# Kernel optimization log

Hardware: AMD Instinct MI355X
Metric: run time of the kernel (lower is better)

## Reference

```python
import jax, jax.numpy as jnp
import numpy as np
from jax import lax

B, L, F, D_MODEL = 4, 256, 80, 2048
ED, N, DT_RANK, K, NL = 4096, 16, 2, 4, 6  # d_inner, d_state, dt_rank, d_conv, n_layers


def setup_inputs():
    key = jax.random.key(0)
    ks = jax.random.split(key, 12)
    rn = lambda k, shp, s=0.02: jax.random.normal(k, shp, dtype=jnp.float32) * s
    return {
        "x": jax.random.normal(ks[0], (B, F, L), dtype=jnp.float32),
        "W_emb": rn(ks[1], (F, D_MODEL)),
        "b_emb": jnp.zeros((D_MODEL,), jnp.float32),
        "norm_w": jnp.ones((NL, D_MODEL), jnp.float32),
        "W_in": rn(ks[2], (NL, D_MODEL, 2 * ED)),
        "b_in": jnp.zeros((NL, 2 * ED), jnp.float32),
        "conv_w": rn(ks[3], (NL, ED, K), 0.1),
        "conv_b": jnp.zeros((NL, ED), jnp.float32),
        "W_x": rn(ks[4], (NL, ED, DT_RANK + 2 * N)),
        "W_dt": rn(ks[5], (NL, DT_RANK, ED), 0.1),
        "b_dt": jnp.full((NL, ED), -4.0, jnp.float32),
        "A_log": jnp.tile(jnp.log(jnp.arange(1, N + 1, dtype=jnp.float32))[None, None, :], (NL, ED, 1)),
        "Dp": jnp.ones((NL, ED), jnp.float32),
        "W_out": rn(ks[6], (NL, ED, D_MODEL)),
        "b_out": jnp.zeros((NL, D_MODEL), jnp.float32),
        "W_f": rn(ks[7], (D_MODEL, 1024)),
        "b_f": jnp.zeros((1024,), jnp.float32),
        "W_h1": rn(ks[8], (1024, 512), 0.05),
        "b_h1": jnp.zeros((512,), jnp.float32),
        "W_h2": rn(ks[9], (512, 256), 0.05),
        "b_h2": jnp.zeros((256,), jnp.float32),
        "W_h3": rn(ks[10], (256, 1), 0.05),
        "b_h3": jnp.zeros((1,), jnp.float32),
    }


def _rmsnorm(x, w, eps=1e-5):
    return x * lax.rsqrt(jnp.mean(x * x, axis=-1, keepdims=True) + eps) * w


def _mamba_block(u, W_in, b_in, conv_w, conv_b, W_x, W_dt, b_dt, A_log, Dp, W_out, b_out):
    xz = u @ W_in + b_in                        # (B,L,2*ED)
    xp, z = jnp.split(xz, 2, axis=-1)
    # causal depthwise conv over time, kernel K
    xc = lax.conv_general_dilated(
        xp.transpose(0, 2, 1), conv_w[:, None, :],
        window_strides=(1,), padding=[(K - 1, 0)],
        feature_group_count=ED,
        dimension_numbers=("NCH", "OIH", "NCH")).transpose(0, 2, 1) + conv_b
    xa = jax.nn.silu(xc)                        # (B,L,ED)
    dbc = xa @ W_x                              # (B,L,dt_rank+2N)
    dt = jax.nn.softplus(dbc[..., :DT_RANK] @ W_dt + b_dt)   # (B,L,ED)
    Bm = dbc[..., DT_RANK:DT_RANK + N]
    Cm = dbc[..., DT_RANK + N:]
    A = -jnp.exp(A_log)                         # (ED,N), negative

    def step(h, inp):
        xa_t, dt_t, B_t, C_t = inp
        h = jnp.exp(dt_t[:, :, None] * A) * h + (dt_t * xa_t)[:, :, None] * B_t[:, None, :]
        return h, jnp.einsum("ben,bn->be", h, C_t)

    step = jax.checkpoint(step)
    h0 = jnp.zeros((xa.shape[0], ED, N), xa.dtype)
    _, ys = lax.scan(step, h0, (xa.transpose(1, 0, 2), dt.transpose(1, 0, 2),
                                Bm.transpose(1, 0, 2), Cm.transpose(1, 0, 2)))
    y = ys.transpose(1, 0, 2) + Dp * xa
    y = y * jax.nn.silu(z)
    return y @ W_out + b_out


def reference(x, W_emb, b_emb, norm_w, W_in, b_in, conv_w, conv_b, W_x, W_dt, b_dt, A_log, Dp, W_out, b_out, W_f, b_f, W_h1, b_h1, W_h2, b_h2, W_h3, b_h3):
    h = x.transpose(0, 2, 1) @ W_emb + b_emb    # (B,L,D_MODEL)
    for i in range(NL):
        h = h + _mamba_block(_rmsnorm(h, norm_w[i]), W_in[i], b_in[i], conv_w[i], conv_b[i],
                             W_x[i], W_dt[i], b_dt[i], A_log[i], Dp[i], W_out[i], b_out[i])
    f = h[:, -1] @ W_f + b_f                    # (B,1024)
    g = jax.nn.silu(f @ W_h1 + b_h1)
    g = g @ W_h2 + b_h2
    g = jnp.where(g > 0, g, 0.01 * g)           # LeakyReLU(0.01)
    return jax.nn.sigmoid(g @ W_h3 + b_h3)      # (B,1)
```

## Files before the change

kernel.cpp:

```cpp
#include <hip/hip_runtime.h>
#include <hip/hip_bf16.h>
#include <math.h>

#define D_MODEL 2048
#define EDIM    4096
#define NSTATE  16
#define LSEQ    256
#define BATCH   4
#define NLAYER  6
#define FDIM    80

typedef __attribute__((ext_vector_type(8))) short bf16x8;
typedef __attribute__((ext_vector_type(4))) float f32x4;

__device__ __forceinline__ float silu_f(float x) { return x / (1.f + __expf(-x)); }

__device__ __forceinline__ float softplus_f(float v) {
  return (v > 20.f) ? v : __logf(1.f + __expf(v));
}

__device__ __forceinline__ unsigned short f2bf(float f) {
  unsigned u = __float_as_uint(f);
  unsigned r = u + 0x7fffu + ((u >> 16) & 1u);
  return (unsigned short)(r >> 16);
}

__device__ __forceinline__ float bf2f(unsigned short u) {
  return __uint_as_float((unsigned)u << 16);
}

__device__ __forceinline__ void gload_lds16(const void* g, void* l) {
  __builtin_amdgcn_global_load_lds(
      (const __attribute__((address_space(1))) unsigned int*)g,
      (__attribute__((address_space(3))) unsigned int*)l, 16, 0, 0);
}

__global__ __launch_bounds__(256) void embed_kernel(
    const float* __restrict__ x, const float* __restrict__ W,
    const float* __restrict__ bias, float* __restrict__ h)
{
  int col = blockIdx.x * 256 + threadIdx.x;
  int row = blockIdx.y;
  int b = row >> 8, l = row & 255;
  const float* xp = x + (size_t)b * FDIM * LSEQ + l;
  float acc = bias[col];
  #pragma unroll 8
  for (int f = 0; f < FDIM; ++f)
    acc = fmaf(xp[(size_t)f * LSEQ], W[(size_t)f * D_MODEL + col], acc);
  h[(size_t)row * D_MODEL + col] = acc;
}

__global__ __launch_bounds__(256) void rmsnorm_kernel(
    const float* __restrict__ h, const float* __restrict__ w, unsigned short* __restrict__ u)
{
  int row = blockIdx.x;
  const float* hr = h + (size_t)row * D_MODEL;
  float s = 0.f;
  for (int i = threadIdx.x; i < D_MODEL; i += 256) { float v = hr[i]; s = fmaf(v, v, s); }
  #pragma unroll
  for (int o = 32; o > 0; o >>= 1) s += __shfl_down(s, o);
  __shared__ float red[4];
  int lane = threadIdx.x & 63, wid = threadIdx.x >> 6;
  if (lane == 0) red[wid] = s;
  __syncthreads();
  float total = red[0] + red[1] + red[2] + red[3];
  float scale = rsqrtf(total * (1.f / D_MODEL) + 1e-5f);
  unsigned short* ur = u + (size_t)row * D_MODEL;
  for (int i = threadIdx.x; i < D_MODEL; i += 256) ur[i] = f2bf(hr[i] * scale * w[i]);
}

__global__ __launch_bounds__(256) void wtrans_kernel(
    const float* __restrict__ W, unsigned short* __restrict__ WT, int K, int N)
{
  __shared__ float t[64][65];
  const int k0 = blockIdx.y * 64, n0 = blockIdx.x * 64;
  const int tc = (threadIdx.x & 15) << 2;
  const int tr = threadIdx.x >> 4;
  #pragma unroll
  for (int i = 0; i < 4; ++i) {
    int r = tr + (i << 4);
    float4 v = *(const float4*)(W + (size_t)(k0 + r) * N + n0 + tc);
    t[r][tc + 0] = v.x; t[r][tc + 1] = v.y; t[r][tc + 2] = v.z; t[r][tc + 3] = v.w;
  }
  __syncthreads();
  #pragma unroll
  for (int i = 0; i < 4; ++i) {
    int rr = tr + (i << 4);
    ushort4 o;
    o.x = f2bf(t[tc + 0][rr]);
    o.y = f2bf(t[tc + 1][rr]);
    o.z = f2bf(t[tc + 2][rr]);
    o.w = f2bf(t[tc + 3][rr]);
    *(ushort4*)(WT + (size_t)(n0 + rr) * K + k0 + tc) = o;
  }
}

__global__ __launch_bounds__(256) void wxt_kernel(
    const float* __restrict__ Wx, float* __restrict__ WxT)
{
  const int e = blockIdx.x * 256 + threadIdx.x;
  const int j = blockIdx.y;
  const int l = blockIdx.z;
  WxT[((size_t)l * 34 + j) * EDIM + e] = Wx[(size_t)l * EDIM * 34 + (size_t)e * 34 + j];
}

template<int BN>
__global__ __launch_bounds__(256) void gemm_bf16(
    const unsigned short* __restrict__ A, int lda,
    const unsigned short* __restrict__ BT, int ldb,
    const float* bias,
    const float* resid, int ldr,
    float* __restrict__ C, int ldc, int K)
{
  constexpr int BM = 128;
  constexpr int FN = BN / 32;
  __shared__ unsigned short As[2][BM * 32];
  __shared__ unsigned short Bs[2][BN * 32];
  const int tid  = threadIdx.x;
  const int wave = tid >> 6;
  const int lane = tid & 63;

  const int nwg = gridDim.x * gridDim.y;
  const int cpx = nwg >> 3;
  int flat = blockIdx.y * gridDim.x + blockIdx.x;
  flat = (flat & 7) * cpx + (flat >> 3);
  const int bm = (flat / gridDim.x) * BM;
  const int bn = (flat % gridDim.x) * BN;

  const int wr = (wave >> 1) * 64;
  const int wc = (wave & 1) * (BN / 2);
  const int srow = lane >> 2;
  const int scol = (lane & 3) * 8;

  auto stage = [&](int buf, int k0) {
    #pragma unroll
    for (int i = 0; i < BM / 64; ++i) {
      int c = wave + i * 4;
      gload_lds16(A + (size_t)(bm + c * 16 + srow) * lda + k0 + scol, &As[buf][c * 512]);
    }
    #pragma unroll
    for (int i = 0; i < BN / 64; ++i) {
      int c = wave + i * 4;
      gload_lds16(BT + (size_t)(bn + c * 16 + srow) * ldb + k0 + scol, &Bs[buf][c * 512]);
    }
  };

  f32x4 acc[4][FN];
  #pragma unroll
  for (int m = 0; m < 4; ++m)
    #pragma unroll
    for (int n = 0; n < FN; ++n)
      acc[m][n] = (f32x4){0.f, 0.f, 0.f, 0.f};

  stage(0, 0);
  const int nk = K >> 5;
  for (int t = 0; t < nk; ++t) {
    const int cur = t & 1;
    __syncthreads();
    if (t + 1 < nk) stage(cur ^ 1, (t + 1) << 5);
    bf16x8 af[4], bfr[FN];
    #pragma unroll
    for (int m = 0; m < 4; ++m)
      af[m] = *(const bf16x8*)&As[cur][(wr + m * 16 + (lane & 15)) * 32 + (lane >> 4) * 8];
    #pragma unroll
    for (int n = 0; n < FN; ++n)
      bfr[n] = *(const bf16x8*)&Bs[cur][(wc + n * 16 + (lane & 15)) * 32 + (lane >> 4) * 8];
    #pragma unroll
    for (int m = 0; m < 4; ++m)
      #pragma unroll
      for (int n = 0; n < FN; ++n)
        acc[m][n] = __builtin_amdgcn_mfma_f32_16x16x32_bf16(af[m], bfr[n], acc[m][n], 0, 0, 0);
  }

  const int rbase = (lane >> 4) * 4;
  const int cbase = lane & 15;
  #pragma unroll
  for (int m = 0; m < 4; ++m) {
    #pragma unroll
    for (int n = 0; n < FN; ++n) {
      const int col = bn + wc + n * 16 + cbase;
      const float bv = bias ? bias[col] : 0.f;
      #pragma unroll
      for (int r = 0; r < 4; ++r) {
        const int row = bm + wr + m * 16 + rbase + r;
        float v = acc[m][n][r] + bv;
        if (resid) v += resid[(size_t)row * ldr + col];
        C[(size_t)row * ldc + col] = v;
      }
    }
  }
}

__global__ __launch_bounds__(256) void conv_dbc_kernel(
    const float* __restrict__ xz, const float* __restrict__ cw,
    const float* __restrict__ cb, const float* __restrict__ WxT,
    unsigned short* __restrict__ xab, float* __restrict__ dbc)
{
  const int row = blockIdx.x;
  const int l = row & (LSEQ - 1);
  const int tid = threadIdx.x;
  float a[16];
  const float* base_row = xz + (size_t)row * 8192;
  #pragma unroll
  for (int k = 0; k < 16; ++k) {
    const int e = k * 256 + tid;
    float4 w = *(const float4*)(cw + (size_t)e * 4);
    const float* base = base_row + e;
    float v = cb[e];
    v = fmaf(w.w, base[0], v);
    if (l >= 1) v = fmaf(w.z, base[-8192], v);
    if (l >= 2) v = fmaf(w.y, base[-2 * 8192], v);
    if (l >= 3) v = fmaf(w.x, base[-3 * 8192], v);
    v = silu_f(v);
    a[k] = v;
    xab[(size_t)row * EDIM + e] = f2bf(v);
  }
  __shared__ float red[34][4];
  const int lane = tid & 63, wid = tid >> 6;
  #pragma unroll
  for (int j = 0; j < 34; ++j) {
    const float* wr = WxT + (size_t)j * EDIM + tid;
    float s = 0.f;
    #pragma unroll
    for (int k = 0; k < 16; ++k)
      s = fmaf(a[k], wr[k * 256], s);
    #pragma unroll
    for (int o = 32; o > 0; o >>= 1) s += __shfl_down(s, o);
    if (lane == 0) red[j][wid] = s;
  }
  __syncthreads();
  if (tid < 34)
    dbc[(size_t)row * 34 + tid] = red[tid][0] + red[tid][1] + red[tid][2] + red[tid][3];
}

struct ScanIn { float x[4], z[4], d0[4], d1[4], B0[4], B1[4], C0[4], C1[4]; };

__device__ __forceinline__ void scan_step(
    const ScanIn& s, float& h0, float& h1,
    float w0, float w1, float bde, float Aa0, float Aa1, float dpe,
    int g, unsigned short* yp, int t0)
{
  #pragma unroll
  for (int u = 0; u < 4; ++u) {
    float v = fmaf(s.d1[u], w1, fmaf(s.d0[u], w0, bde));
    float dta = softplus_f(v);
    float dtxa = dta * s.x[u];
    h0 = fmaf(__expf(dta * Aa0), h0, dtxa * s.B0[u]);
    h1 = fmaf(__expf(dta * Aa1), h1, dtxa * s.B1[u]);
    float part = fmaf(h0, s.C0[u], h1 * s.C1[u]);
    part += __shfl_xor(part, 8);
    part += __shfl_xor(part, 16);
    part += __shfl_xor(part, 32);
    if (g == 0) {
      float yv = fmaf(dpe, s.x[u], part);
      yp[(size_t)(t0 + u) * EDIM] = f2bf(yv * silu_f(s.z[u]));
    }
  }
}

__global__ __launch_bounds__(256) void scan_kernel(
    const unsigned short* __restrict__ xab, const float* __restrict__ xz,
    const float* __restrict__ dbc,
    const float* __restrict__ Wdt, const float* __restrict__ bdt,
    const float* __restrict__ Alog, const float* __restrict__ Dpp,
    unsigned short* __restrict__ ybf)
{
  __shared__ unsigned short sx[256 * 32];
  __shared__ unsigned short sz[256 * 32];
  __shared__ float          sd01[256 * 2];
  __shared__ unsigned short sBC[256 * 32];

  const int tid = threadIdx.x;
  const int b = blockIdx.x >> 7;
  const int chunk = blockIdx.x & 127;
  const int wave = tid >> 6;
  const int lane = tid & 63;
  const int ch = lane & 7;
  const int g = lane >> 3;
  const int we = wave * 8 + ch;
  const int e = chunk * 32 + we;

  const unsigned short* xsrc = xab + (size_t)(b << 8) * EDIM + chunk * 32;
  const float* zsrc = xz + (size_t)(b << 8) * 8192 + EDIM + chunk * 32;
  const float* dsrc = dbc + (size_t)(b << 8) * 34;
  #pragma unroll
  for (int i = 0; i < 8; ++i) {
    int idx = i * 256 + tid;
    int t = idx >> 3, q = idx & 7;
    *(ushort4*)&sx[t * 32 + q * 4] = *(const ushort4*)&xsrc[(size_t)t * EDIM + q * 4];
    float4 v = *(const float4*)&zsrc[(size_t)t * 8192 + q * 4];
    ushort4 o; o.x = f2bf(v.x); o.y = f2bf(v.y); o.z = f2bf(v.z); o.w = f2bf(v.w);
    *(ushort4*)&sz[t * 32 + q * 4] = o;
  }
  {
    float2 v = *(const float2*)&dsrc[(size_t)tid * 34];
    *(float2*)&sd01[tid * 2] = v;
  }
  #pragma unroll
  for (int i = 0; i < 16; ++i) {
    int idx = i * 256 + tid;
    int t = idx >> 4, q = idx & 15;
    float2 v = *(const float2*)&dsrc[(size_t)t * 34 + 2 + q * 2];
    ushort2 o; o.x = f2bf(v.x); o.y = f2bf(v.y);
    *(ushort2*)&sBC[t * 32 + q * 2] = o;
  }
  __syncthreads();

  const float w0 = Wdt[e], w1 = Wdt[EDIM + e], bde = bdt[e];
  const float Aa0 = -__expf(Alog[(size_t)e * 16 + g * 2]);
  const float Aa1 = -__expf(Alog[(size_t)e * 16 + g * 2 + 1]);
  const float dpe = Dpp[e];
  float h0 = 0.f, h1 = 0.f;
  unsigned short* yp = ybf + (size_t)(b << 8) * EDIM + e;

  auto load = [&](ScanIn& s, int t0) {
    #pragma unroll
    for (int u = 0; u < 4; ++u) {
      const int t = t0 + u;
      s.x[u]  = bf2f(sx[t * 32 + we]);
      s.z[u]  = bf2f(sz[t * 32 + we]);
      s.d0[u] = sd01[t * 2];
      s.d1[u] = sd01[t * 2 + 1];
      s.B0[u] = bf2f(sBC[t * 32 + 2 * g]);
      s.B1[u] = bf2f(sBC[t * 32 + 2 * g + 1]);
      s.C0[u] = bf2f(sBC[t * 32 + 16 + 2 * g]);
      s.C1[u] = bf2f(sBC[t * 32 + 16 + 2 * g + 1]);
    }
  };

  ScanIn sa, sb;
  load(sa, 0);
  for (int t0 = 0; t0 < LSEQ; t0 += 8) {
    load(sb, t0 + 4);
    scan_step(sa, h0, h1, w0, w1, bde, Aa0, Aa1, dpe, g, yp, t0);
    if (t0 + 8 < LSEQ) load(sa, t0 + 8);
    scan_step(sb, h0, h1, w0, w1, bde, Aa0, Aa1, dpe, g, yp, t0 + 4);
  }
}

template<int KS>
__global__ __launch_bounds__(256) void head_gemm_part(
    const float* __restrict__ in, int in_stride,
    const float* __restrict__ W, int N,
    float* __restrict__ part)
{
  const int j = blockIdx.x * 256 + threadIdx.x;
  const int b = blockIdx.y;
  const int s = blockIdx.z;
  const int k0 = s * KS;
  __shared__ float sIn[KS];
  if (threadIdx.x < KS) sIn[threadIdx.x] = in[(size_t)b * in_stride + k0 + threadIdx.x];
  __syncthreads();
  float acc = 0.f;
  #pragma unroll 8
  for (int k = 0; k < KS; ++k)
    acc = fmaf(sIn[k], W[(size_t)(k0 + k) * N + j], acc);
  part[((size_t)s * gridDim.y + b) * N + j] = acc;
}

__global__ __launch_bounds__(256) void head_reduce(
    const float* __restrict__ part, const float* __restrict__ bias,
    float* __restrict__ outp, int N, int S, int act)
{
  const int j = blockIdx.x * 256 + threadIdx.x;
  const int b = blockIdx.y;
  const int B = gridDim.y;
  float acc = bias[j];
  for (int s = 0; s < S; ++s)
    acc += part[((size_t)s * B + b) * N + j];
  if (act == 1) acc = silu_f(acc);
  else if (act == 2) acc = (acc > 0.f) ? acc : 0.01f * acc;
  outp[(size_t)b * N + j] = acc;
}

__global__ __launch_bounds__(256) void head_final_kernel(
    const float* __restrict__ g2, const float* __restrict__ W,
    const float* __restrict__ bb, float* __restrict__ out)
{
  int b_idx = threadIdx.x >> 6;
  int lane = threadIdx.x & 63;
  float s = 0.f;
  #pragma unroll
  for (int i = 0; i < 4; ++i) {
    int k = lane + i * 64;
    s = fmaf(g2[b_idx * 256 + k], W[k], s);
  }
  #pragma unroll
  for (int o = 32; o > 0; o >>= 1) s += __shfl_down(s, o);
  if (lane == 0) out[b_idx] = 1.f / (1.f + __expf(-(s + bb[0])));
}

extern "C" void kernel_launch(void* const* d_in, const int* in_sizes, int n_in,
                              void* d_out, int out_size, void* d_ws, size_t ws_size,
                              hipStream_t stream)
{
  const float* x      = (const float*)d_in[0];
  const float* W_emb  = (const float*)d_in[1];
  const float* b_emb  = (const float*)d_in[2];
  const float* norm_w = (const float*)d_in[3];
  const float* W_in   = (const float*)d_in[4];
  const float* b_in   = (const float*)d_in[5];
  const float* conv_w = (const float*)d_in[6];
  const float* conv_b = (const float*)d_in[7];
  const float* W_x    = (const float*)d_in[8];
  const float* W_dt   = (const float*)d_in[9];
  const float* b_dt   = (const float*)d_in[10];
  const float* A_log  = (const float*)d_in[11];
  const float* Dp     = (const float*)d_in[12];
  const float* W_out  = (const float*)d_in[13];
  const float* b_out  = (const float*)d_in[14];
  const float* W_f    = (const float*)d_in[15];
  const float* b_f    = (const float*)d_in[16];
  const float* W_h1   = (const float*)d_in[17];
  const float* b_h1   = (const float*)d_in[18];
  const float* W_h2   = (const float*)d_in[19];
  const float* b_h2   = (const float*)d_in[20];
  const float* W_h3   = (const float*)d_in[21];
  const float* b_h3   = (const float*)d_in[22];
  float* out = (float*)d_out;

  char* ws = (char*)d_ws;
  float*          hA  = (float*)ws;                 ws += (size_t)1024 * 2048 * 4;
  float*          hB  = (float*)ws;                 ws += (size_t)1024 * 2048 * 4;
  unsigned short* ubf = (unsigned short*)ws;        ws += (size_t)1024 * 2048 * 2;
  float*          xz  = (float*)ws;                 ws += (size_t)1024 * 8192 * 4;
  unsigned short* xab = (unsigned short*)ws;        ws += (size_t)1024 * 4096 * 2;
  float*          dbc = (float*)ws;                 ws += (size_t)1024 * 40 * 4;
  unsigned short* ybf = (unsigned short*)ws;        ws += (size_t)1024 * 4096 * 2;
  unsigned short* WT  = (unsigned short*)ws;        ws += (size_t)8192 * 2048 * 2;
  float*          WxT = (float*)ws;                 ws += (size_t)NLAYER * 34 * EDIM * 4;
  float*          part= (float*)ws;                 ws += (size_t)16 * 4 * 1024 * 4;
  float*          fb  = (float*)ws;                 ws += 4096 * 4;
  float*          g1b = (float*)ws;                 ws += 2048 * 4;
  float*          g2b = (float*)ws;                 ws += 1024 * 4;

  embed_kernel<<<dim3(D_MODEL / 256, 1024), 256, 0, stream>>>(x, W_emb, b_emb, hA);
  wxt_kernel<<<dim3(EDIM / 256, 34, NLAYER), 256, 0, stream>>>(W_x, WxT);

  float* hin = hA;
  float* hout = hB;
  for (int i = 0; i < NLAYER; ++i) {
    const float* Wi  = W_in  + (size_t)i * 2048 * 8192;
    const float* bi  = b_in  + (size_t)i * 8192;
    const float* cwi = conv_w + (size_t)i * 4096 * 4;
    const float* cbi = conv_b + (size_t)i * 4096;
    const float* Wdti= W_dt  + (size_t)i * 2 * 4096;
    const float* bdti= b_dt  + (size_t)i * 4096;
    const float* Ali = A_log + (size_t)i * 4096 * 16;
    const float* Dpi = Dp    + (size_t)i * 4096;
    const float* Woi = W_out + (size_t)i * 4096 * 2048;
    const float* boi = b_out + (size_t)i * 2048;
    const float* nwi = norm_w + (size_t)i * 2048;

    rmsnorm_kernel<<<1024, 256, 0, stream>>>(hin, nwi, ubf);
    wtrans_kernel<<<dim3(8192 / 64, 2048 / 64), 256, 0, stream>>>(Wi, WT, 2048, 8192);
    gemm_bf16<128><<<dim3(8192 / 128, 1024 / 128), 256, 0, stream>>>(
        ubf, 2048, WT, 2048, bi, nullptr, 0, xz, 8192, 2048);
    conv_dbc_kernel<<<1024, 256, 0, stream>>>(
        xz, cwi, cbi, WxT + (size_t)i * 34 * EDIM, xab, dbc);
    scan_kernel<<<512, 256, 0, stream>>>(xab, xz, dbc, Wdti, bdti, Ali, Dpi, ybf);
    wtrans_kernel<<<dim3(2048 / 64, 4096 / 64), 256, 0, stream>>>(Woi, WT, 4096, 2048);
    gemm_bf16<64><<<dim3(2048 / 64, 1024 / 128), 256, 0, stream>>>(
        ybf, 4096, WT, 4096, boi, hin, 2048, hout, 2048, 4096);
    float* tmp = hin; hin = hout; hout = tmp;
  }

  head_gemm_part<128><<<dim3(1024 / 256, BATCH, 16), 256, 0, stream>>>(
      hin + (size_t)255 * 2048, 256 * 2048, W_f, 1024, part);
  head_reduce<<<dim3(1024 / 256, BATCH), 256, 0, stream>>>(part, b_f, fb, 1024, 16, 0);
  head_gemm_part<128><<<dim3(512 / 256, BATCH, 8), 256, 0, stream>>>(
      fb, 1024, W_h1, 512, part);
  head_reduce<<<dim3(512 / 256, BATCH), 256, 0, stream>>>(part, b_h1, g1b, 512, 8, 1);
  head_gemm_part<128><<<dim3(256 / 256, BATCH, 4), 256, 0, stream>>>(
      g1b, 512, W_h2, 256, part);
  head_reduce<<<dim3(256 / 256, BATCH), 256, 0, stream>>>(part, b_h2, g2b, 256, 4, 2);
  head_final_kernel<<<1, 256, 0, stream>>>(g2b, W_h3, b_h3, out);
}
```

Measured before the change: 1.783 ms.

## Split selective scan into chunked three-pass parallel scan over time

Replaces the single sequential scan kernel, which walked all 256 timesteps per block, with three kernels. The first computes each 32-step chunk's local state and summed dt, the second does a short prefix combine across 8 chunks to seed each chunk's initial state, and the third replays each chunk from its seed to produce outputs. This exposes 8x more blocks, shortening the serial dependency chain and raising GPU occupancy. The cost is recomputing the recurrence twice, two extra launches, and extra global traffic for the partial states and seeds.

Result: slower. 1.833 ms, median of 5 (+2.8%).

```diff
diff --git a/kernel.cpp b/kernel.cpp
--- a/kernel.cpp
+++ b/kernel.cpp
@@ -9,6 +9,8 @@
 #define BATCH   4
 #define NLAYER  6
 #define FDIM    80
+#define TCH     32
+#define NCH     8
 
 typedef __attribute__((ext_vector_type(8))) short bf16x8;
 typedef __attribute__((ext_vector_type(4))) float f32x4;
@@ -233,74 +235,134 @@
     dbc[(size_t)row * 34 + tid] = red[tid][0] + red[tid][1] + red[tid][2] + red[tid][3];
 }
 
-struct ScanIn { float x[4], z[4], d0[4], d1[4], B0[4], B1[4], C0[4], C1[4]; };
-
-__device__ __forceinline__ void scan_step(
-    const ScanIn& s, float& h0, float& h1,
-    float w0, float w1, float bde, float Aa0, float Aa1, float dpe,
-    int g, unsigned short* yp, int t0)
-{
-  #pragma unroll
-  for (int u = 0; u < 4; ++u) {
-    float v = fmaf(s.d1[u], w1, fmaf(s.d0[u], w0, bde));
-    float dta = softplus_f(v);
-    float dtxa = dta * s.x[u];
-    h0 = fmaf(__expf(dta * Aa0), h0, dtxa * s.B0[u]);
-    h1 = fmaf(__expf(dta * Aa1), h1, dtxa * s.B1[u]);
-    float part = fmaf(h0, s.C0[u], h1 * s.C1[u]);
-    part += __shfl_xor(part, 8);
-    part += __shfl_xor(part, 16);
-    part += __shfl_xor(part, 32);
-    if (g == 0) {
-      float yv = fmaf(dpe, s.x[u], part);
-      yp[(size_t)(t0 + u) * EDIM] = f2bf(yv * silu_f(s.z[u]));
-    }
-  }
-}
-
-__global__ __launch_bounds__(256) void scan_kernel(
-    const unsigned short* __restrict__ xab, const float* __restrict__ xz,
-    const float* __restrict__ dbc,
+
+__global__ __launch_bounds__(256) void scan_part_kernel(
+    const unsigned short* __restrict__ xab, const float* __restrict__ dbc,
     const float* __restrict__ Wdt, const float* __restrict__ bdt,
-    const float* __restrict__ Alog, const float* __restrict__ Dpp,
-    unsigned short* __restrict__ ybf)
-{
-  __shared__ unsigned short sx[256 * 32];
-  __shared__ unsigned short sz[256 * 32];
-  __shared__ float          sd01[256 * 2];
-  __shared__ unsigned short sBC[256 * 32];
+    const float* __restrict__ Alog,
+    float* __restrict__ hpart, float* __restrict__ Spart)
+{
+  __shared__ unsigned short sx[TCH * 32];
+  __shared__ float          sd01[TCH * 2];
+  __shared__ unsigned short sBC[TCH * 32];
 
   const int tid = threadIdx.x;
   const int b = blockIdx.x >> 7;
   const int chunk = blockIdx.x & 127;
+  const int tc = blockIdx.y;
   const int wave = tid >> 6;
   const int lane = tid & 63;
   const int ch = lane & 7;
   const int g = lane >> 3;
   const int we = wave * 8 + ch;
   const int e = chunk * 32 + we;
-
-  const unsigned short* xsrc = xab + (size_t)(b << 8) * EDIM + chunk * 32;
-  const float* zsrc = xz + (size_t)(b << 8) * 8192 + EDIM + chunk * 32;
+  const int row0 = (b << 8) + tc * TCH;
+
+  const unsigned short* xsrc = xab + (size_t)row0 * EDIM + chunk * 32;
   const float* dsrc = dbc + (size_t)(b << 8) * 34;
-  #pragma unroll
-  for (int i = 0; i < 8; ++i) {
+  {
+    int t = tid >> 3, q = tid & 7;
+    *(ushort4*)&sx[t * 32 + q * 4] = *(const ushort4*)&xsrc[(size_t)t * EDIM + q * 4];
+  }
+  if (tid < TCH) {
+    float2 v = *(const float2*)&dsrc[(size_t)(tc * TCH + tid) * 34];
+    *(float2*)&sd01[tid * 2] = v;
+  }
+  #pragma unroll
+  for (int i = 0; i < 2; ++i) {
     int idx = i * 256 + tid;
-    int t = idx >> 3, q = idx & 7;
+    int t = idx >> 4, q = idx & 15;
+    float2 v = *(const float2*)&dsrc[(size_t)(tc * TCH + t) * 34 + 2 + q * 2];
+    ushort2 o; o.x = f2bf(v.x); o.y = f2bf(v.y);
+    *(ushort2*)&sBC[t * 32 + q * 2] = o;
+  }
+  __syncthreads();
+
+  const float w0 = Wdt[e], w1 = Wdt[EDIM + e], bde = bdt[e];
+  const float Aa0 = -__expf(Alog[(size_t)e * 16 + g * 2]);
+  const float Aa1 = -__expf(Alog[(size_t)e * 16 + g * 2 + 1]);
+  float h0 = 0.f, h1 = 0.f, S = 0.f;
+
+  #pragma unroll 4
+  for (int t = 0; t < TCH; ++t) {
+    float d0 = sd01[t * 2], d1 = sd01[t * 2 + 1];
+    float v = fmaf(d1, w1, fmaf(d0, w0, bde));
+    float dta = softplus_f(v);
+    S += dta;
+    float xv = bf2f(sx[t * 32 + we]);
+    float dtxa = dta * xv;
+    h0 = fmaf(__expf(dta * Aa0), h0, dtxa * bf2f(sBC[t * 32 + 2 * g]));
+    h1 = fmaf(__expf(dta * Aa1), h1, dtxa * bf2f(sBC[t * 32 + 2 * g + 1]));
+  }
+
+  const size_t base = ((size_t)(b * NCH + tc) * EDIM + e);
+  hpart[base * 16 + g * 2]     = h0;
+  hpart[base * 16 + g * 2 + 1] = h1;
+  if (g == 0) Spart[base] = S;
+}
+
+__global__ __launch_bounds__(256) void scan_prefix_kernel(
+    const float* __restrict__ hpart, const float* __restrict__ Spart,
+    const float* __restrict__ Alog, float* __restrict__ seed)
+{
+  const int id = blockIdx.x * 256 + threadIdx.x;
+  const int n = id & 15;
+  const int e = (id >> 4) & 4095;
+  const int b = id >> 16;
+  const float Aa = -__expf(Alog[(size_t)e * 16 + n]);
+  float H = 0.f;
+  #pragma unroll
+  for (int c = 0; c < NCH; ++c) {
+    const size_t base = ((size_t)(b * NCH + c) * EDIM + e);
+    seed[base * 16 + n] = H;
+    float a = __expf(Aa * Spart[base]);
+    H = fmaf(a, H, hpart[base * 16 + n]);
+  }
+}
+
+__global__ __launch_bounds__(256) void scan_final_kernel(
+    const unsigned short* __restrict__ xab, const float* __restrict__ xz,
+    const float* __restrict__ dbc, const float* __restrict__ seed,
+    const float* __restrict__ Wdt, const float* __restrict__ bdt,
+    const float* __restrict__ Alog, const float* __restrict__ Dpp,
+    unsigned short* __restrict__ ybf)
+{
+  __shared__ unsigned short sx[TCH * 32];
+  __shared__ unsigned short sz[TCH * 32];
+  __shared__ float          sd01[TCH * 2];
+  __shared__ unsigned short sBC[TCH * 32];
+
+  const int tid = threadIdx.x;
+  const int b = blockIdx.x >> 7;
+  const int chunk = blockIdx.x & 127;
+  const int tc = blockIdx.y;
+  const int wave = tid >> 6;
+  const int lane = tid & 63;
+  const int ch = lane & 7;
+  const int g = lane >> 3;
+  const int we = wave * 8 + ch;
+  const int e = chunk * 32 + we;
+  const int row0 = (b << 8) + tc * TCH;
+
+  const unsigned short* xsrc = xab + (size_t)row0 * EDIM + chunk * 32;
+  const float* zsrc = xz + (size_t)row0 * 8192 + EDIM + chunk * 32;
+  const float* dsrc = dbc + (size_t)(b << 8) * 34;
+  {
+    int t = tid >> 3, q = tid & 7;
     *(ushort4*)&sx[t * 32 + q * 4] = *(const ushort4*)&xsrc[(size_t)t * EDIM + q * 4];
     float4 v = *(const float4*)&zsrc[(size_t)t * 8192 + q * 4];
     ushort4 o; o.x = f2bf(v.x); o.y = f2bf(v.y); o.z = f2bf(v.z); o.w = f2bf(v.w);
     *(ushort4*)&sz[t * 32 + q * 4] = o;
   }
-  {
-    float2 v = *(const float2*)&dsrc[(size_t)tid * 34];
+  if (tid < TCH) {
+    float2 v = *(const float2*)&dsrc[(size_t)(tc * TCH + tid) * 34];
     *(float2*)&sd01[tid * 2] = v;
   }
   #pragma unroll
-  for (int i = 0; i < 16; ++i) {
+  for (int i = 0; i < 2; ++i) {
     int idx = i * 256 + tid;
     int t = idx >> 4, q = idx & 15;
-    float2 v = *(const float2*)&dsrc[(size_t)t * 34 + 2 + q * 2];
+    float2 v = *(const float2*)&dsrc[(size_t)(tc * TCH + t) * 34 + 2 + q * 2];
     ushort2 o; o.x = f2bf(v.x); o.y = f2bf(v.y);
     *(ushort2*)&sBC[t * 32 + q * 2] = o;
   }
@@ -310,31 +372,29 @@
   const float Aa0 = -__expf(Alog[(size_t)e * 16 + g * 2]);
   const float Aa1 = -__expf(Alog[(size_t)e * 16 + g * 2 + 1]);
   const float dpe = Dpp[e];
-  float h0 = 0.f, h1 = 0.f;
-  unsigned short* yp = ybf + (size_t)(b << 8) * EDIM + e;
-
-  auto load = [&](ScanIn& s, int t0) {
-    #pragma unroll
-    for (int u = 0; u < 4; ++u) {
-      const int t = t0 + u;
-      s.x[u]  = bf2f(sx[t * 32 + we]);
-      s.z[u]  = bf2f(sz[t * 32 + we]);
-      s.d0[u] = sd01[t * 2];
-      s.d1[u] = sd01[t * 2 + 1];
-      s.B0[u] = bf2f(sBC[t * 32 + 2 * g]);
-      s.B1[u] = bf2f(sBC[t * 32 + 2 * g + 1]);
-      s.C0[u] = bf2f(sBC[t * 32 + 16 + 2 * g]);
-      s.C1[u] = bf2f(sBC[t * 32 + 16 + 2 * g + 1]);
+  const size_t sbase = ((size_t)(b * NCH + tc) * EDIM + e) * 16;
+  float h0 = seed[sbase + g * 2];
+  float h1 = seed[sbase + g * 2 + 1];
+  unsigned short* yp = ybf + (size_t)row0 * EDIM + e;
+
+  #pragma unroll 4
+  for (int t = 0; t < TCH; ++t) {
+    float d0 = sd01[t * 2], d1 = sd01[t * 2 + 1];
+    float v = fmaf(d1, w1, fmaf(d0, w0, bde));
+    float dta = softplus_f(v);
+    float xv = bf2f(sx[t * 32 + we]);
+    float dtxa = dta * xv;
+    h0 = fmaf(__expf(dta * Aa0), h0, dtxa * bf2f(sBC[t * 32 + 2 * g]));
+    h1 = fmaf(__expf(dta * Aa1), h1, dtxa * bf2f(sBC[t * 32 + 2 * g + 1]));
+    float part = fmaf(h0, bf2f(sBC[t * 32 + 16 + 2 * g]),
+                      h1 * bf2f(sBC[t * 32 + 16 + 2 * g + 1]));
+    part += __shfl_xor(part, 8);
+    part += __shfl_xor(part, 16);
+    part += __shfl_xor(part, 32);
+    if (g == 0) {
+      float yv = fmaf(dpe, xv, part);
+      yp[(size_t)t * EDIM] = f2bf(yv * silu_f(bf2f(sz[t * 32 + we])));
     }
-  };
-
-  ScanIn sa, sb;
-  load(sa, 0);
-  for (int t0 = 0; t0 < LSEQ; t0 += 8) {
-    load(sb, t0 + 4);
-    scan_step(sa, h0, h1, w0, w1, bde, Aa0, Aa1, dpe, g, yp, t0);
-    if (t0 + 8 < LSEQ) load(sa, t0 + 8);
-    scan_step(sb, h0, h1, w0, w1, bde, Aa0, Aa1, dpe, g, yp, t0 + 4);
   }
 }
 
@@ -420,19 +480,22 @@
   float* out = (float*)d_out;
 
   char* ws = (char*)d_ws;
-  float*          hA  = (float*)ws;                 ws += (size_t)1024 * 2048 * 4;
-  float*          hB  = (float*)ws;                 ws += (size_t)1024 * 2048 * 4;
-  unsigned short* ubf = (unsigned short*)ws;        ws += (size_t)1024 * 2048 * 2;
-  float*          xz  = (float*)ws;                 ws += (size_t)1024 * 8192 * 4;
-  unsigned short* xab = (unsigned short*)ws;        ws += (size_t)1024 * 4096 * 2;
-  float*          dbc = (float*)ws;                 ws += (size_t)1024 * 40 * 4;
-  unsigned short* ybf = (unsigned short*)ws;        ws += (size_t)1024 * 4096 * 2;
-  unsigned short* WT  = (unsigned short*)ws;        ws += (size_t)8192 * 2048 * 2;
-  float*          WxT = (float*)ws;                 ws += (size_t)NLAYER * 34 * EDIM * 4;
-  float*          part= (float*)ws;                 ws += (size_t)16 * 4 * 1024 * 4;
-  float*          fb  = (float*)ws;                 ws += 4096 * 4;
-  float*          g1b = (float*)ws;                 ws += 2048 * 4;
-  float*          g2b = (float*)ws;                 ws += 1024 * 4;
+  float*          hA   = (float*)ws;                ws += (size_t)1024 * 2048 * 4;
+  float*          hB   = (float*)ws;                ws += (size_t)1024 * 2048 * 4;
+  unsigned short* ubf  = (unsigned short*)ws;       ws += (size_t)1024 * 2048 * 2;
+  float*          xz   = (float*)ws;                ws += (size_t)1024 * 8192 * 4;
+  unsigned short* xab  = (unsigned short*)ws;       ws += (size_t)1024 * 4096 * 2;
+  float*          dbc  = (float*)ws;                ws += (size_t)1024 * 40 * 4;
+  unsigned short* ybf  = (unsigned short*)ws;       ws += (size_t)1024 * 4096 * 2;
+  unsigned short* WT   = (unsigned short*)ws;       ws += (size_t)8192 * 2048 * 2;
+  float*          WxT  = (float*)ws;                ws += (size_t)NLAYER * 34 * EDIM * 4;
+  float*          hpart= (float*)ws;                ws += (size_t)BATCH * NCH * EDIM * 16 * 4;
+  float*          Spart= (float*)ws;                ws += (size_t)BATCH * NCH * EDIM * 4;
+  float*          seed = (float*)ws;                ws += (size_t)BATCH * NCH * EDIM * 16 * 4;
+  float*          part = (float*)ws;                ws += (size_t)16 * 4 * 1024 * 4;
+  float*          fb   = (float*)ws;                ws += 4096 * 4;
+  float*          g1b  = (float*)ws;                ws += 2048 * 4;
+  float*          g2b  = (float*)ws;                ws += 1024 * 4;
 
   embed_kernel<<<dim3(D_MODEL / 256, 1024), 256, 0, stream>>>(x, W_emb, b_emb, hA);
   wxt_kernel<<<dim3(EDIM / 256, 34, NLAYER), 256, 0, stream>>>(W_x, WxT);
@@ -458,7 +521,12 @@
         ubf, 2048, WT, 2048, bi, nullptr, 0, xz, 8192, 2048);
     conv_dbc_kernel<<<1024, 256, 0, stream>>>(
         xz, cwi, cbi, WxT + (size_t)i * 34 * EDIM, xab, dbc);
-    scan_kernel<<<512, 256, 0, stream>>>(xab, xz, dbc, Wdti, bdti, Ali, Dpi, ybf);
+    scan_part_kernel<<<dim3(512, NCH), 256, 0, stream>>>(
+        xab, dbc, Wdti, bdti, Ali, hpart, Spart);
+    scan_prefix_kernel<<<(BATCH * EDIM * 16) / 256, 256, 0, stream>>>(
+        hpart, Spart, Ali, seed);
+    scan_final_kernel<<<dim3(512, NCH), 256, 0, stream>>>(
+        xab, xz, dbc, seed, Wdti, bdti, Ali, Dpi, ybf);
     wtrans_kernel<<<dim3(2048 / 64, 4096 / 64), 256, 0, stream>>>(Woi, WT, 4096, 2048);
     gemm_bf16<64><<<dim3(2048 / 64, 1024 / 128), 256, 0, stream>>>(
         ybf, 4096, WT, 4096, boi, hin, 2048, hout, 2048, 4096);
```
